# Kernel optimization log

Hardware: AMD Instinct MI355X
Metric: run time of the kernel (lower is better)

## Reference

```python
import jax, jax.numpy as jnp
import numpy as np

IN_FEATURES = 1024
OUT_FEATURES = 1024
NUM_GMM = 5
MAX_STD = 3.0
ROWS = (IN_FEATURES + 1) * OUT_FEATURES  # (in+1)*out rows of GMM params


def setup_inputs() -> dict:
    key = jax.random.key(0)
    kx, km, kl, kw = jax.random.split(key, 4)
    x = jax.random.normal(kx, (4096, IN_FEATURES), dtype=jnp.float32)
    mean = jax.random.normal(km, (ROWS, NUM_GMM), dtype=jnp.float32)
    logstd = jax.random.normal(kl, (ROWS, NUM_GMM), dtype=jnp.float32)
    weight = jax.random.normal(kw, (ROWS, NUM_GMM), dtype=jnp.float32)
    return {"x": x, "mean": mean, "logstd": logstd, "weight": weight}


def reference(x, mean, logstd, weight):
    # GMM weight sampling: Categorical(softmax(weight)) picks a component per row,
    # then Normal(mean_sel, exp(tanh(logstd_sel)*max_std)) is sampled.
    key = jax.random.key(42)
    kcat, knorm = jax.random.split(key)
    # categorical with logits == Categorical(probs=softmax(weight))
    idx = jax.random.categorical(kcat, weight, axis=-1)  # [ROWS] int
    sel_mean = jnp.take_along_axis(mean, idx[:, None], axis=1)[:, 0]      # [ROWS]
    sel_logstd = jnp.take_along_axis(logstd, idx[:, None], axis=1)[:, 0]  # [ROWS]
    sel_std = jnp.exp(jnp.tanh(sel_logstd) * MAX_STD)
    eps = jax.random.normal(knorm, (mean.shape[0],), dtype=mean.dtype)
    weight_bias = sel_mean + sel_std * eps  # torch .sample() -> no grad flow
    weight_bias = jax.lax.stop_gradient(weight_bias)
    bias = weight_bias[:OUT_FEATURES]                                   # [out]
    W = weight_bias[OUT_FEATURES:].reshape(OUT_FEATURES, IN_FEATURES)   # [out, in]
    return x @ W.T + bias
```

## Files before the change

kernel.cpp:

```cpp
#include <hip/hip_runtime.h>
#include <cstdint>
#include <cmath>

#define IN_FEATURES 1024
#define OUT_FEATURES 1024
#define NUM_GMM 5
#define ROWS ((IN_FEATURES + 1) * OUT_FEATURES)

struct U2 { uint32_t a, b; };

__host__ __device__ constexpr uint32_t rotl32c(uint32_t x, int d) {
  return (x << d) | (x >> (32 - d));
}

#define TF_ROUND(r) { x0 += x1; x1 = rotl32c(x1, (r)); x1 ^= x0; }
__host__ __device__ constexpr U2 threefry2x32(uint32_t k0, uint32_t k1,
                                              uint32_t x0, uint32_t x1) {
  const uint32_t ks0 = k0, ks1 = k1, ks2 = k0 ^ k1 ^ 0x1BD11BDAu;
  x0 += ks0; x1 += ks1;
  TF_ROUND(13) TF_ROUND(15) TF_ROUND(26) TF_ROUND(6)
  x0 += ks1; x1 += ks2 + 1u;
  TF_ROUND(17) TF_ROUND(29) TF_ROUND(16) TF_ROUND(24)
  x0 += ks2; x1 += ks0 + 2u;
  TF_ROUND(13) TF_ROUND(15) TF_ROUND(26) TF_ROUND(6)
  x0 += ks0; x1 += ks1 + 3u;
  TF_ROUND(17) TF_ROUND(29) TF_ROUND(16) TF_ROUND(24)
  x0 += ks1; x1 += ks2 + 4u;
  TF_ROUND(13) TF_ROUND(15) TF_ROUND(26) TF_ROUND(6)
  x0 += ks2; x1 += ks0 + 5u;
  return U2{x0, x1};
}

constexpr U2 KC = threefry2x32(0u, 42u, 0u, 0u);
constexpr U2 KN = threefry2x32(0u, 42u, 0u, 1u);
constexpr uint32_t KCAT0  = KC.a;
constexpr uint32_t KCAT1  = KC.b;
constexpr uint32_t KNORM0 = KN.a;
constexpr uint32_t KNORM1 = KN.b;

__device__ inline float u01_from_bits(uint32_t bits) {
  return __uint_as_float((bits >> 9) | 0x3F800000u) - 1.0f;
}

__device__ inline float log_f32_acc(float x) {
  uint32_t ix = __float_as_uint(x);
  int e = (int)(ix >> 23) - 127;
  float mf = __uint_as_float((ix & 0x007FFFFFu) | 0x3F800000u);
  if (mf > 1.4142135381698608f) { mf *= 0.5f; e += 1; }
  double m = (double)mf;
  double t = (m - 1.0) / (m + 1.0);
  double t2 = t * t;
  double p = 1.0 / 15.0;
  p = fma(p, t2, 1.0 / 13.0);
  p = fma(p, t2, 1.0 / 11.0);
  p = fma(p, t2, 1.0 / 9.0);
  p = fma(p, t2, 1.0 / 7.0);
  p = fma(p, t2, 1.0 / 5.0);
  p = fma(p, t2, 1.0 / 3.0);
  p = fma(p, t2, 1.0);
  double r = fma((double)e, 0.693147180559945309417, 2.0 * t * p);
  return (float)r;
}

__device__ inline float gumbel_from_bits(uint32_t bits) {
  float f = u01_from_bits(bits);
  float u = fmaxf(1.17549435e-38f, f + 1.17549435e-38f);
  float t1 = log_f32_acc(u);
  float t2 = log_f32_acc(-t1);
  return -t2;
}

__device__ inline float erfinv_xla(float x) {
  float w = -log1pf(-x * x);
  float p;
  if (w < 5.0f) {
    w = w - 2.5f;
    p = 2.81022636e-08f;
    p = fmaf(p, w, 3.43273939e-07f);
    p = fmaf(p, w, -3.5233877e-06f);
    p = fmaf(p, w, -4.39150654e-06f);
    p = fmaf(p, w, 0.00021858087f);
    p = fmaf(p, w, -0.00125372503f);
    p = fmaf(p, w, -0.00417768164f);
    p = fmaf(p, w, 0.246640727f);
    p = fmaf(p, w, 1.50140941f);
  } else {
    w = sqrtf(w) - 3.0f;
    p = -0.000200214257f;
    p = fmaf(p, w, 0.000100950558f);
    p = fmaf(p, w, 0.00134934322f);
    p = fmaf(p, w, -0.00367342844f);
    p = fmaf(p, w, 0.00573950773f);
    p = fmaf(p, w, -0.0076224613f);
    p = fmaf(p, w, 0.00943887047f);
    p = fmaf(p, w, 1.00167406f);
    p = fmaf(p, w, 2.83297682f);
  }
  return p * x;
}

__device__ inline float normal_from_bits(uint32_t bits) {
  float f = u01_from_bits(bits);
  const float lo = -0.99999994f;
  float u = fmaxf(lo, f * 2.0f + lo);
  return 1.4142135623730951f * erfinv_xla(u);
}

__device__ inline unsigned short f32_to_bf16_rne(float f) {
  uint32_t u = __float_as_uint(f);
  return (unsigned short)((u + 0x7FFFu + ((u >> 16) & 1u)) >> 16);
}

__global__ __launch_bounds__(256) void gmm_sample_kernel(
    const float* __restrict__ mean, const float* __restrict__ logstd,
    const float* __restrict__ weight, unsigned short* __restrict__ wh,
    float* __restrict__ bias_f32) {
  int r = blockIdx.x * blockDim.x + threadIdx.x;
  if (r >= ROWS) return;

  const float* wrow = weight + (size_t)r * NUM_GMM;
  int idx = 0;
  float best = -3.402823466e+38f;
#pragma unroll
  for (int g = 0; g < NUM_GMM; ++g) {
    U2 t = threefry2x32(KCAT0, KCAT1, 0u, (uint32_t)(r * NUM_GMM + g));
    float v = gumbel_from_bits(t.a ^ t.b) + wrow[g];
    if (v > best) { best = v; idx = g; }
  }

  U2 tn = threefry2x32(KNORM0, KNORM1, 0u, (uint32_t)r);
  float eps = normal_from_bits(tn.a ^ tn.b);

  float m = mean[(size_t)r * NUM_GMM + idx];
  float l = logstd[(size_t)r * NUM_GMM + idx];
  float sd = expf(tanhf(l) * 3.0f);
  float wbv = m + sd * eps;
  wh[r] = f32_to_bf16_rne(wbv);
  if (r < OUT_FEATURES) bias_f32[r] = wbv;
}

__global__ __launch_bounds__(256) void convert_x_kernel(
    const float* __restrict__ x, unsigned short* __restrict__ xh) {
  int i = (blockIdx.x * 256 + threadIdx.x) * 8;
  float4 a = *(const float4*)(x + i);
  float4 b = *(const float4*)(x + i + 4);
  union { unsigned short s[8]; uint4 v; } o;
  o.s[0] = f32_to_bf16_rne(a.x); o.s[1] = f32_to_bf16_rne(a.y);
  o.s[2] = f32_to_bf16_rne(a.z); o.s[3] = f32_to_bf16_rne(a.w);
  o.s[4] = f32_to_bf16_rne(b.x); o.s[5] = f32_to_bf16_rne(b.y);
  o.s[6] = f32_to_bf16_rne(b.z); o.s[7] = f32_to_bf16_rne(b.w);
  *(uint4*)(xh + i) = o.v;
}

typedef __attribute__((ext_vector_type(8))) short bf16x8;
typedef __attribute__((ext_vector_type(4))) float f32x4;

#define GBM 128
#define GBN 64
#define GBK 32

__device__ inline void load_lds16(const void* g, void* l) {
  __builtin_amdgcn_global_load_lds(
      (const __attribute__((address_space(1))) unsigned int*)g,
      (__attribute__((address_space(3))) unsigned int*)l, 16, 0, 0);
}

__global__ __launch_bounds__(256) void gemm_mfma_kernel(
    const unsigned short* __restrict__ xh, const unsigned short* __restrict__ wh,
    const float* __restrict__ bias, float* __restrict__ out) {
  __shared__ unsigned short As[GBM * GBK];
  __shared__ unsigned short Bs[GBN * GBK];

  const unsigned short* W = wh + OUT_FEATURES;
  const int tid = threadIdx.x;
  const int w = tid >> 6;
  const int L = tid & 63;

  const int m_tile = blockIdx.y * GBM;
  const int n_tile = blockIdx.x * GBN;

  const int sm = tid & 15;
  const int sh = (tid >> 4) & 3;
  const int sb = tid >> 6;

  const unsigned short* gA0 = xh + (size_t)(m_tile + sb * 16 + sm) * IN_FEATURES + 8 * sh;
  const unsigned short* gA1 = xh + (size_t)(m_tile + (sb + 4) * 16 + sm) * IN_FEATURES + 8 * sh;
  const unsigned short* gB  = W  + (size_t)(n_tile + sb * 16 + sm) * IN_FEATURES + 8 * sh;

  f32x4 acc[4][2];
#pragma unroll
  for (int f = 0; f < 4; ++f)
#pragma unroll
    for (int j = 0; j < 2; ++j) acc[f][j] = (f32x4){0.f, 0.f, 0.f, 0.f};

  const int aoff = (w >> 1) * 4 * 512 + L * 8;
  const int boff = (w & 1) * 2 * 512 + L * 8;

  for (int k0 = 0; k0 < IN_FEATURES; k0 += GBK) {
    load_lds16(gA0 + k0, As + (size_t)tid * 8);
    load_lds16(gA1 + k0, As + (size_t)(256 + tid) * 8);
    load_lds16(gB + k0,  Bs + (size_t)tid * 8);
    __syncthreads();

    bf16x8 a0 = *(const bf16x8*)(As + aoff);
    bf16x8 a1 = *(const bf16x8*)(As + aoff + 512);
    bf16x8 a2 = *(const bf16x8*)(As + aoff + 1024);
    bf16x8 a3 = *(const bf16x8*)(As + aoff + 1536);
    bf16x8 b0 = *(const bf16x8*)(Bs + boff);
    bf16x8 b1 = *(const bf16x8*)(Bs + boff + 512);

    acc[0][0] = __builtin_amdgcn_mfma_f32_16x16x32_bf16(a0, b0, acc[0][0], 0, 0, 0);
    acc[0][1] = __builtin_amdgcn_mfma_f32_16x16x32_bf16(a0, b1, acc[0][1], 0, 0, 0);
    acc[1][0] = __builtin_amdgcn_mfma_f32_16x16x32_bf16(a1, b0, acc[1][0], 0, 0, 0);
    acc[1][1] = __builtin_amdgcn_mfma_f32_16x16x32_bf16(a1, b1, acc[1][1], 0, 0, 0);
    acc[2][0] = __builtin_amdgcn_mfma_f32_16x16x32_bf16(a2, b0, acc[2][0], 0, 0, 0);
    acc[2][1] = __builtin_amdgcn_mfma_f32_16x16x32_bf16(a2, b1, acc[2][1], 0, 0, 0);
    acc[3][0] = __builtin_amdgcn_mfma_f32_16x16x32_bf16(a3, b0, acc[3][0], 0, 0, 0);
    acc[3][1] = __builtin_amdgcn_mfma_f32_16x16x32_bf16(a3, b1, acc[3][1], 0, 0, 0);
    __syncthreads();
  }

  const int col_base = n_tile + (w & 1) * 32 + (L & 15);
  const int row_base = m_tile + (w >> 1) * 64 + (L >> 4) * 4;
  float bv0 = bias[col_base];
  float bv1 = bias[col_base + 16];
#pragma unroll
  for (int f = 0; f < 4; ++f) {
#pragma unroll
    for (int reg = 0; reg < 4; ++reg) {
      int row = row_base + f * 16 + reg;
      out[(size_t)row * OUT_FEATURES + col_base]      = acc[f][0][reg] + bv0;
      out[(size_t)row * OUT_FEATURES + col_base + 16] = acc[f][1][reg] + bv1;
    }
  }
}

extern "C" void kernel_launch(void* const* d_in, const int* in_sizes, int n_in,
                              void* d_out, int out_size, void* d_ws, size_t ws_size,
                              hipStream_t stream) {
  const float* x      = (const float*)d_in[0];
  const float* mean   = (const float*)d_in[1];
  const float* logstd = (const float*)d_in[2];
  const float* weight = (const float*)d_in[3];
  float* out = (float*)d_out;

  const int M = in_sizes[0] / IN_FEATURES;

  unsigned short* xh = (unsigned short*)d_ws;
  unsigned short* wh = (unsigned short*)((char*)d_ws + (size_t)M * IN_FEATURES * 2);
  float* biasf = (float*)((char*)wh + (size_t)ROWS * 2);

  gmm_sample_kernel<<<(ROWS + 255) / 256, 256, 0, stream>>>(
      mean, logstd, weight, wh, biasf);

  convert_x_kernel<<<(M * IN_FEATURES) / (256 * 8), 256, 0, stream>>>(x, xh);

  dim3 grid(OUT_FEATURES / GBN, M / GBM);
  gemm_mfma_kernel<<<grid, 256, 0, stream>>>(xh, wh, biasf, out);
}
```

Baseline: 151.3 us.

## Fuse sampling and x conversion, double-buffer GEMM with BK=64, cheaper transcendental math

The GMM sampling kernel and the x-to-bf16 conversion are merged into one prep launch, removing a kernel launch and its serialization. The GEMM now uses a K tile of 64 with double-buffered LDS. Each K step's loads for the next tile are issued before computing the current one, which halves the barrier count and overlaps global loads with MFMA. Each wave now computes a 32x64 sub-tile. The log helper replaces the double division with an rcp plus Newton refinement, and tanh/exp use fast __expf and rcp, which may change sample bits slightly versus the reference.

```diff
diff --git a/kernel.cpp b/kernel.cpp
--- a/kernel.cpp
+++ b/kernel.cpp
@@ -48,7 +48,11 @@
   float mf = __uint_as_float((ix & 0x007FFFFFu) | 0x3F800000u);
   if (mf > 1.4142135381698608f) { mf *= 0.5f; e += 1; }
   double m = (double)mf;
-  double t = (m - 1.0) / (m + 1.0);
+  double d = m + 1.0;
+  double r = (double)__builtin_amdgcn_rcpf((float)d);
+  r = r * (2.0 - d * r);
+  r = r * (2.0 - d * r);
+  double t = (m - 1.0) * r;
   double t2 = t * t;
   double p = 1.0 / 15.0;
   p = fma(p, t2, 1.0 / 13.0);
@@ -58,8 +62,8 @@
   p = fma(p, t2, 1.0 / 5.0);
   p = fma(p, t2, 1.0 / 3.0);
   p = fma(p, t2, 1.0);
-  double r = fma((double)e, 0.693147180559945309417, 2.0 * t * p);
-  return (float)r;
+  double res = fma((double)e, 0.693147180559945309417, 2.0 * t * p);
+  return (float)res;
 }
 
 __device__ inline float gumbel_from_bits(uint32_t bits) {
@@ -111,12 +115,24 @@
   return (unsigned short)((u + 0x7FFFu + ((u >> 16) & 1u)) >> 16);
 }
 
-__global__ __launch_bounds__(256) void gmm_sample_kernel(
+__global__ __launch_bounds__(256) void prep_kernel(
     const float* __restrict__ mean, const float* __restrict__ logstd,
-    const float* __restrict__ weight, unsigned short* __restrict__ wh,
-    float* __restrict__ bias_f32) {
-  int r = blockIdx.x * blockDim.x + threadIdx.x;
-  if (r >= ROWS) return;
+    const float* __restrict__ weight, const float* __restrict__ x,
+    unsigned short* __restrict__ wh, float* __restrict__ bias_f32,
+    unsigned short* __restrict__ xh, int n_chunks) {
+  const int r = blockIdx.x * 256 + threadIdx.x;
+
+  if (r < n_chunks) {
+    int i = r * 8;
+    float4 a = *(const float4*)(x + i);
+    float4 b = *(const float4*)(x + i + 4);
+    union { unsigned short s[8]; uint4 v; } o;
+    o.s[0] = f32_to_bf16_rne(a.x); o.s[1] = f32_to_bf16_rne(a.y);
+    o.s[2] = f32_to_bf16_rne(a.z); o.s[3] = f32_to_bf16_rne(a.w);
+    o.s[4] = f32_to_bf16_rne(b.x); o.s[5] = f32_to_bf16_rne(b.y);
+    o.s[6] = f32_to_bf16_rne(b.z); o.s[7] = f32_to_bf16_rne(b.w);
+    *(uint4*)(xh + i) = o.v;
+  }
 
   const float* wrow = weight + (size_t)r * NUM_GMM;
   int idx = 0;
@@ -133,31 +149,20 @@
 
   float m = mean[(size_t)r * NUM_GMM + idx];
   float l = logstd[(size_t)r * NUM_GMM + idx];
-  float sd = expf(tanhf(l) * 3.0f);
+  float e2 = __expf(2.0f * l);
+  float th = 1.0f - 2.0f * __builtin_amdgcn_rcpf(e2 + 1.0f);
+  float sd = __expf(3.0f * th);
   float wbv = m + sd * eps;
   wh[r] = f32_to_bf16_rne(wbv);
   if (r < OUT_FEATURES) bias_f32[r] = wbv;
 }
 
-__global__ __launch_bounds__(256) void convert_x_kernel(
-    const float* __restrict__ x, unsigned short* __restrict__ xh) {
-  int i = (blockIdx.x * 256 + threadIdx.x) * 8;
-  float4 a = *(const float4*)(x + i);
-  float4 b = *(const float4*)(x + i + 4);
-  union { unsigned short s[8]; uint4 v; } o;
-  o.s[0] = f32_to_bf16_rne(a.x); o.s[1] = f32_to_bf16_rne(a.y);
-  o.s[2] = f32_to_bf16_rne(a.z); o.s[3] = f32_to_bf16_rne(a.w);
-  o.s[4] = f32_to_bf16_rne(b.x); o.s[5] = f32_to_bf16_rne(b.y);
-  o.s[6] = f32_to_bf16_rne(b.z); o.s[7] = f32_to_bf16_rne(b.w);
-  *(uint4*)(xh + i) = o.v;
-}
-
 typedef __attribute__((ext_vector_type(8))) short bf16x8;
 typedef __attribute__((ext_vector_type(4))) float f32x4;
 
 #define GBM 128
 #define GBN 64
-#define GBK 32
+#define GBK 64
 
 __device__ inline void load_lds16(const void* g, void* l) {
   __builtin_amdgcn_global_load_lds(
@@ -168,8 +173,8 @@
 __global__ __launch_bounds__(256) void gemm_mfma_kernel(
     const unsigned short* __restrict__ xh, const unsigned short* __restrict__ wh,
     const float* __restrict__ bias, float* __restrict__ out) {
-  __shared__ unsigned short As[GBM * GBK];
-  __shared__ unsigned short Bs[GBN * GBK];
+  __shared__ unsigned short As[2][GBM * GBK];
+  __shared__ unsigned short Bs[2][GBN * GBK];
 
   const unsigned short* W = wh + OUT_FEATURES;
   const int tid = threadIdx.x;
@@ -181,56 +186,77 @@
 
   const int sm = tid & 15;
   const int sh = (tid >> 4) & 3;
-  const int sb = tid >> 6;
-
-  const unsigned short* gA0 = xh + (size_t)(m_tile + sb * 16 + sm) * IN_FEATURES + 8 * sh;
-  const unsigned short* gA1 = xh + (size_t)(m_tile + (sb + 4) * 16 + sm) * IN_FEATURES + 8 * sh;
-  const unsigned short* gB  = W  + (size_t)(n_tile + sb * 16 + sm) * IN_FEATURES + 8 * sh;
-
-  f32x4 acc[4][2];
-#pragma unroll
-  for (int f = 0; f < 4; ++f)
-#pragma unroll
-    for (int j = 0; j < 2; ++j) acc[f][j] = (f32x4){0.f, 0.f, 0.f, 0.f};
-
-  const int aoff = (w >> 1) * 4 * 512 + L * 8;
-  const int boff = (w & 1) * 2 * 512 + L * 8;
-
-  for (int k0 = 0; k0 < IN_FEATURES; k0 += GBK) {
-    load_lds16(gA0 + k0, As + (size_t)tid * 8);
-    load_lds16(gA1 + k0, As + (size_t)(256 + tid) * 8);
-    load_lds16(gB + k0,  Bs + (size_t)tid * 8);
+  const int sk = (tid >> 6) & 1;
+  const int sb = tid >> 7;
+  const int kofs = sk * 32 + sh * 8;
+
+  const unsigned short* gA[4];
+  const unsigned short* gB[2];
+#pragma unroll
+  for (int i = 0; i < 4; ++i)
+    gA[i] = xh + (size_t)(m_tile + (2 * i + sb) * 16 + sm) * IN_FEATURES + kofs;
+#pragma unroll
+  for (int i = 0; i < 2; ++i)
+    gB[i] = W + (size_t)(n_tile + (2 * i + sb) * 16 + sm) * IN_FEATURES + kofs;
+
+  f32x4 acc[2][4];
+#pragma unroll
+  for (int a = 0; a < 2; ++a)
+#pragma unroll
+    for (int b = 0; b < 4; ++b) acc[a][b] = (f32x4){0.f, 0.f, 0.f, 0.f};
+
+#define STAGE(buf, k0)                                                    \
+  {                                                                       \
+    _Pragma("unroll")                                                     \
+    for (int i = 0; i < 4; ++i)                                           \
+      load_lds16(gA[i] + (k0), &As[buf][(size_t)(tid + 256 * i) * 8]);    \
+    _Pragma("unroll")                                                     \
+    for (int i = 0; i < 2; ++i)                                           \
+      load_lds16(gB[i] + (k0), &Bs[buf][(size_t)(tid + 256 * i) * 8]);    \
+  }
+
+  STAGE(0, 0)
+
+  const int NK = IN_FEATURES / GBK;
+  for (int kt = 0; kt < NK; ++kt) {
     __syncthreads();
-
-    bf16x8 a0 = *(const bf16x8*)(As + aoff);
-    bf16x8 a1 = *(const bf16x8*)(As + aoff + 512);
-    bf16x8 a2 = *(const bf16x8*)(As + aoff + 1024);
-    bf16x8 a3 = *(const bf16x8*)(As + aoff + 1536);
-    bf16x8 b0 = *(const bf16x8*)(Bs + boff);
-    bf16x8 b1 = *(const bf16x8*)(Bs + boff + 512);
-
-    acc[0][0] = __builtin_amdgcn_mfma_f32_16x16x32_bf16(a0, b0, acc[0][0], 0, 0, 0);
-    acc[0][1] = __builtin_amdgcn_mfma_f32_16x16x32_bf16(a0, b1, acc[0][1], 0, 0, 0);
-    acc[1][0] = __builtin_amdgcn_mfma_f32_16x16x32_bf16(a1, b0, acc[1][0], 0, 0, 0);
-    acc[1][1] = __builtin_amdgcn_mfma_f32_16x16x32_bf16(a1, b1, acc[1][1], 0, 0, 0);
-    acc[2][0] = __builtin_amdgcn_mfma_f32_16x16x32_bf16(a2, b0, acc[2][0], 0, 0, 0);
-    acc[2][1] = __builtin_amdgcn_mfma_f32_16x16x32_bf16(a2, b1, acc[2][1], 0, 0, 0);
-    acc[3][0] = __builtin_amdgcn_mfma_f32_16x16x32_bf16(a3, b0, acc[3][0], 0, 0, 0);
-    acc[3][1] = __builtin_amdgcn_mfma_f32_16x16x32_bf16(a3, b1, acc[3][1], 0, 0, 0);
-    __syncthreads();
-  }
-
-  const int col_base = n_tile + (w & 1) * 32 + (L & 15);
-  const int row_base = m_tile + (w >> 1) * 64 + (L >> 4) * 4;
-  float bv0 = bias[col_base];
-  float bv1 = bias[col_base + 16];
-#pragma unroll
-  for (int f = 0; f < 4; ++f) {
+    if (kt + 1 < NK) STAGE((kt + 1) & 1, (kt + 1) * GBK)
+    const unsigned short* Ab = As[kt & 1];
+    const unsigned short* Bb = Bs[kt & 1];
+#pragma unroll
+    for (int s = 0; s < 2; ++s) {
+      bf16x8 a0 = *(const bf16x8*)(Ab + (((2 * w + 0) * 2 + s) * 64 + L) * 8);
+      bf16x8 a1 = *(const bf16x8*)(Ab + (((2 * w + 1) * 2 + s) * 64 + L) * 8);
+      bf16x8 b0 = *(const bf16x8*)(Bb + ((0 * 2 + s) * 64 + L) * 8);
+      bf16x8 b1 = *(const bf16x8*)(Bb + ((1 * 2 + s) * 64 + L) * 8);
+      bf16x8 b2 = *(const bf16x8*)(Bb + ((2 * 2 + s) * 64 + L) * 8);
+      bf16x8 b3 = *(const bf16x8*)(Bb + ((3 * 2 + s) * 64 + L) * 8);
+      acc[0][0] = __builtin_amdgcn_mfma_f32_16x16x32_bf16(a0, b0, acc[0][0], 0, 0, 0);
+      acc[0][1] = __builtin_amdgcn_mfma_f32_16x16x32_bf16(a0, b1, acc[0][1], 0, 0, 0);
+      acc[0][2] = __builtin_amdgcn_mfma_f32_16x16x32_bf16(a0, b2, acc[0][2], 0, 0, 0);
+      acc[0][3] = __builtin_amdgcn_mfma_f32_16x16x32_bf16(a0, b3, acc[0][3], 0, 0, 0);
+      acc[1][0] = __builtin_amdgcn_mfma_f32_16x16x32_bf16(a1, b0, acc[1][0], 0, 0, 0);
+      acc[1][1] = __builtin_amdgcn_mfma_f32_16x16x32_bf16(a1, b1, acc[1][1], 0, 0, 0);
+      acc[1][2] = __builtin_amdgcn_mfma_f32_16x16x32_bf16(a1, b2, acc[1][2], 0, 0, 0);
+      acc[1][3] = __builtin_amdgcn_mfma_f32_16x16x32_bf16(a1, b3, acc[1][3], 0, 0, 0);
+    }
+  }
+
+  const int colL = L & 15;
+  const int rowq = (L >> 4) * 4;
+  float bv[4];
+#pragma unroll
+  for (int nb = 0; nb < 4; ++nb) bv[nb] = bias[n_tile + nb * 16 + colL];
+#pragma unroll
+  for (int bm = 0; bm < 2; ++bm) {
 #pragma unroll
     for (int reg = 0; reg < 4; ++reg) {
-      int row = row_base + f * 16 + reg;
-      out[(size_t)row * OUT_FEATURES + col_base]      = acc[f][0][reg] + bv0;
-      out[(size_t)row * OUT_FEATURES + col_base + 16] = acc[f][1][reg] + bv1;
+      int row = m_tile + w * 32 + bm * 16 + rowq + reg;
+#pragma unroll
+      for (int nb = 0; nb < 4; ++nb) {
+        out[(size_t)row * OUT_FEATURES + n_tile + nb * 16 + colL] =
+            acc[bm][nb][reg] + bv[nb];
+      }
     }
   }
 }
@@ -250,10 +276,9 @@
   unsigned short* wh = (unsigned short*)((char*)d_ws + (size_t)M * IN_FEATURES * 2);
   float* biasf = (float*)((char*)wh + (size_t)ROWS * 2);
 
-  gmm_sample_kernel<<<(ROWS + 255) / 256, 256, 0, stream>>>(
-      mean, logstd, weight, wh, biasf);
-
-  convert_x_kernel<<<(M * IN_FEATURES) / (256 * 8), 256, 0, stream>>>(x, xh);
+  const int n_chunks = M * IN_FEATURES / 8;
+  prep_kernel<<<ROWS / 256, 256, 0, stream>>>(
+      mean, logstd, weight, x, wh, biasf, xh, n_chunks);
 
   dim3 grid(OUT_FEATURES / GBN, M / GBM);
   gemm_mfma_kernel<<<grid, 256, 0, stream>>>(xh, wh, biasf, out);
```

Result: faster. 144.9 us (-4.2%).
